# Performance work log

Measured on AMD Instinct MI355X. Metric: run time of the kernel, lower is better.

Reference implementation:

```python
import jax, jax.numpy as jnp
import numpy as np

EPS = 1e-5

def layer_norm(x, w, b):
    m = jnp.mean(x, axis=-1, keepdims=True)
    v = jnp.mean(jnp.square(x - m), axis=-1, keepdims=True)
    return (x - m) * jax.lax.rsqrt(v + EPS) * w + b

def setup_inputs() -> dict:
    key = jax.random.key(0)
    B, S, D, H = 4, 2048, 768, 12
    Dh, F = D // H, 4 * D
    ks = jax.random.split(key, 16)
    s = 0.02
    return {
        "x":    jax.random.normal(ks[0], (B, S, D), dtype=jnp.float32),
        # per-head q/k/v projections stacked over heads: [H, D, Dh]
        "Wq":   jax.random.normal(ks[1], (H, D, Dh), dtype=jnp.float32) * s,
        "bq":   jnp.zeros((H, Dh), dtype=jnp.float32),
        "Wk":   jax.random.normal(ks[2], (H, D, Dh), dtype=jnp.float32) * s,
        "bk":   jnp.zeros((H, Dh), dtype=jnp.float32),
        "Wv":   jax.random.normal(ks[3], (H, D, Dh), dtype=jnp.float32) * s,
        "bv":   jnp.zeros((H, Dh), dtype=jnp.float32),
        "Wo":   jax.random.normal(ks[4], (D, D), dtype=jnp.float32) * s,
        "bo":   jnp.zeros((D,), dtype=jnp.float32),
        "W1":   jax.random.normal(ks[5], (D, F), dtype=jnp.float32) * s,
        "b1":   jnp.zeros((F,), dtype=jnp.float32),
        "W2":   jax.random.normal(ks[6], (F, D), dtype=jnp.float32) * s,
        "b2":   jnp.zeros((D,), dtype=jnp.float32),
        "ln1_w": jnp.ones((D,), dtype=jnp.float32),
        "ln1_b": jnp.zeros((D,), dtype=jnp.float32),
        "ln2_w": jnp.ones((D,), dtype=jnp.float32),
        "ln2_b": jnp.zeros((D,), dtype=jnp.float32),
    }

def reference(x, Wq, bq, Wk, bk, Wv, bv, Wo, bo, W1, b1, W2, b2,
              ln1_w, ln1_b, ln2_w, ln2_b):
    B, S, D = x.shape
    H, _, Dh = Wq.shape
    scale = jnp.sqrt(jnp.float32(Dh))  # torch scales by sqrt(dout)
    # q,k,v: [B, H, S, Dh]
    q = jnp.einsum('bsd,hde->bhse', x, Wq) + bq[None, :, None, :]
    k = jnp.einsum('bsd,hde->bhse', x, Wk) + bk[None, :, None, :]
    v = jnp.einsum('bsd,hde->bhse', x, Wv) + bv[None, :, None, :]
    scores = jnp.einsum('bhqe,bhke->bhqk', q, k) / scale  # [B,H,S,S]
    causal = jnp.tril(jnp.ones((S, S), dtype=bool))
    scores = jnp.where(causal[None, None], scores, -jnp.inf)
    attn = jax.nn.softmax(scores, axis=-1)
    ctx = jnp.einsum('bhqk,bhke->bhqe', attn, v)           # [B,H,S,Dh]
    ctx = jnp.transpose(ctx, (0, 2, 1, 3)).reshape(B, S, D)  # concat heads
    att_out = ctx @ Wo + bo
    h = layer_norm(x + att_out, ln1_w, ln1_b)  # post-norm, dropout=0
    ff = jax.nn.gelu(h @ W1 + b1, approximate=False) @ W2 + b2
    return layer_norm(h + ff, ln2_w, ln2_b)
```

## Files before the change

### kernel.cpp

```cpp
#include <hip/hip_runtime.h>
#include <hip/hip_bf16.h>
#include <math.h>

#define B_ 4
#define S_ 2048
#define D_ 768
#define H_ 12
#define DH_ 64
#define F_ 3072
#define NTOK (B_*S_)
#define BH_ (B_*H_)

typedef __hip_bfloat16 bf16;
typedef __attribute__((ext_vector_type(8))) short bf16x8;
typedef __attribute__((ext_vector_type(4))) float f32x4;
typedef __attribute__((ext_vector_type(4))) _Float16 half4;
typedef __attribute__((ext_vector_type(8))) _Float16 half8;

#define GLD16(g, l) __builtin_amdgcn_global_load_lds( \
    (__attribute__((address_space(1))) void*)(uintptr_t)(g), \
    (__attribute__((address_space(3))) void*)(uintptr_t)(l), 16, 0, 0)

__device__ __forceinline__ float bs2f(short s){
  union { unsigned int u; float f; } cv; cv.u = ((unsigned int)(unsigned short)s) << 16; return cv.f;
}
__device__ __forceinline__ float b2f(bf16 v){ return __bfloat162float(v); }
__device__ __forceinline__ bf16 f2b(float v){ return __float2bfloat16(v); }
__device__ __forceinline__ short f2bb(float v){ bf16 b = f2b(v); short s; __builtin_memcpy(&s, &b, 2); return s; }

__device__ __forceinline__ float gelu_fast(float v){
  const float c0 = -2.302208157f;
  const float c1 = -0.102943238f;
  float w = v*v;
  float z = v * __builtin_fmaf(c1, w, c0);
  float t = __builtin_amdgcn_exp2f(z);
  return v * __builtin_amdgcn_rcpf(1.0f + t);
}

__global__ void f32_to_bf16_k(const float* __restrict__ in, bf16* __restrict__ out, int n){
  int i = blockIdx.x*256 + threadIdx.x;
  if (i < n) out[i] = f2b(in[i]);
}

__global__ __launch_bounds__(256) void transpose_f32_bf16_k(const float* __restrict__ in,
    bf16* __restrict__ out, int K, int N){
  __shared__ float t[32][33];
  const int kb = blockIdx.y*32, nb = blockIdx.x*32;
  const int x = threadIdx.x & 31, y = threadIdx.x >> 5;
#pragma unroll
  for (int yy = y; yy < 32; yy += 8)
    t[yy][x] = in[(size_t)(kb+yy)*N + nb + x];
  __syncthreads();
#pragma unroll
  for (int yy = y; yy < 32; yy += 8)
    out[(size_t)(nb+yy)*K + kb + x] = f2b(t[x][yy]);
}

__global__ void pack_qkv_t_k(const float* __restrict__ Wq, const float* __restrict__ bq,
                             const float* __restrict__ Wk, const float* __restrict__ bk,
                             const float* __restrict__ Wv, const float* __restrict__ bv,
                             bf16* __restrict__ Wt, float* __restrict__ bcat){
  int idx = blockIdx.x*256 + threadIdx.x;
  if (idx < 3*D_*D_){
    int n = idx / D_;
    int k = idx - n*D_;
    int which = n / D_;
    int cc = n - which*D_;
    int h = cc >> 6, e = cc & 63;
    const float* W = (which==0) ? Wq : ((which==1) ? Wk : Wv);
    Wt[idx] = f2b(W[((size_t)h*D_ + k)*DH_ + e]);
  }
  if (idx < 3*D_){
    int which = idx / D_;
    int cc = idx - which*D_;
    int h = cc >> 6, e = cc & 63;
    const float* bb = (which==0) ? bq : ((which==1) ? bk : bv);
    bcat[idx] = bb[h*DH_ + e];
  }
}

template<int EPI>
__global__ __launch_bounds__(256) void mgemm_k(
    const bf16* __restrict__ A, const bf16* __restrict__ Bt,
    const float* __restrict__ bias, const bf16* __restrict__ aux,
    bf16* __restrict__ C, int M, int N, int K,
    bf16* __restrict__ qb, bf16* __restrict__ kbuf, _Float16* __restrict__ vt)
{
  __shared__ bf16 As[4096];
  __shared__ bf16 Bs[4096];
  const int tid  = threadIdx.x;
  const int wave = tid >> 6, lane = tid & 63;
  const int quad = lane >> 4, l16 = lane & 15;
  const int wm = (wave >> 1) * 64, wn = (wave & 1) * 64;

  const int NX = gridDim.x;
  const int f  = blockIdx.y * NX + blockIdx.x;
  const int xcd = f & 7;
  const int j   = f >> 3;
  const int bx  = j % NX;
  const int by  = (j / NX) * 8 + xcd;
  const int m0 = by * 128, n0 = bx * 128;

  const int srow  = lane >> 2;
  const int schunk = (lane & 3) ^ ((srow >> 1) & 3);
  const bf16* gA0 = A  + (size_t)(m0 + wave*16 + srow)*K + schunk*8;
  const bf16* gA1 = gA0 + (size_t)64*K;
  const bf16* gB0 = Bt + (size_t)(n0 + wave*16 + srow)*K + schunk*8;
  const bf16* gB1 = gB0 + (size_t)64*K;
  const uintptr_t asb = (uintptr_t)(void*)As + (size_t)wave*1024;
  const uintptr_t bsb = (uintptr_t)(void*)Bs + (size_t)wave*1024;

  f32x4 acc[4][4];
#pragma unroll
  for (int i=0;i<4;i++)
#pragma unroll
    for (int j2=0;j2<4;j2++) acc[i][j2] = (f32x4)0.f;

  const char* AsB = (const char*)As;
  const char* BsB = (const char*)Bs;
  const int fsw = (quad ^ ((l16 >> 1) & 3)) * 16;

  for (int k0 = 0; k0 < K; k0 += 32){
    __syncthreads();
    GLD16(gA0, asb);
    GLD16(gA1, asb + 4096);
    GLD16(gB0, bsb);
    GLD16(gB1, bsb + 4096);
    gA0 += 32; gA1 += 32; gB0 += 32; gB1 += 32;
    __syncthreads();
    bf16x8 af[4], bfr[4];
#pragma unroll
    for (int i=0;i<4;i++) af[i]  = *(const bf16x8*)(AsB + ((wm + i*16 + l16) << 6) + fsw);
#pragma unroll
    for (int j2=0;j2<4;j2++) bfr[j2] = *(const bf16x8*)(BsB + ((wn + j2*16 + l16) << 6) + fsw);
#pragma unroll
    for (int i=0;i<4;i++)
#pragma unroll
      for (int j2=0;j2<4;j2++)
        acc[i][j2] = __builtin_amdgcn_mfma_f32_16x16x32_bf16(af[i], bfr[j2], acc[i][j2], 0, 0, 0);
  }

#pragma unroll
  for (int i=0;i<4;i++){
#pragma unroll
    for (int j2=0;j2<4;j2++){
      const int n = n0 + wn + j2*16 + l16;
      const int m_base = m0 + wm + i*16 + quad*4;
      if (EPI == 0){
        const int which = n / D_;
        const int cc = n - which*D_;
        const int h = cc >> 6, e = cc & 63;
        if (which == 2){
          const int b = m_base >> 11, s = m_base & (S_-1);
          const int sl = s & 63;
          const int perm = ((sl>>2)&3)*16 + ((sl>>4)&3)*4;
          half4 hv;
#pragma unroll
          for (int r=0;r<4;r++) hv[r] = (_Float16)(acc[i][j2][r] + bias[n]);
          *(half4*)(vt + ((size_t)(b*H_+h)*DH_ + e)*S_ + (s & ~63) + perm) = hv;
        } else {
          bf16* dst = (which==0) ? qb : kbuf;
          const float sc2 = (which==0) ? 0.125f : 1.0f;
#pragma unroll
          for (int r=0;r<4;r++){
            const int m = m_base + r;
            const int b = m >> 11, s = m & (S_-1);
            dst[((size_t)(b*H_+h)*S_ + s)*DH_ + e] = f2b((acc[i][j2][r] + bias[n]) * sc2);
          }
        }
      } else {
#pragma unroll
        for (int r=0;r<4;r++){
          const int m = m_base + r;
          float v = acc[i][j2][r] + bias[n];
          if (EPI == 1){
            v += b2f(aux[(size_t)m*N + n]);
            C[(size_t)m*N + n] = f2b(v);
          } else {
            C[(size_t)m*N + n] = f2b(gelu_fast(v));
          }
        }
      }
    }
  }
}

__global__ __launch_bounds__(256) void mgemm64_k(
    const bf16* __restrict__ A, const bf16* __restrict__ Bt,
    const float* __restrict__ bias, const bf16* __restrict__ aux,
    bf16* __restrict__ C, int M, int N, int K)
{
  __shared__ bf16 As[4096];
  __shared__ bf16 Bs[8192];
  const int tid  = threadIdx.x;
  const int wave = tid >> 6, lane = tid & 63;
  const int quad = lane >> 4, l16 = lane & 15;
  const int wm = (wave >> 1) * 32, wn = (wave & 1) * 64;

  const int NX = gridDim.x;
  const int f  = blockIdx.y * NX + blockIdx.x;
  const int xcd = f & 7;
  const int j   = f >> 3;
  const int bx  = j % NX;
  const int by  = (j / NX) * 8 + xcd;
  const int m0 = by * 64, n0 = bx * 128;

  const int srow8 = lane >> 3;
  const int g     = (lane & 7) ^ srow8;
  const bf16* gA0 = A  + (size_t)(m0 + wave*16 +      srow8)*K + g*8;
  const bf16* gA1 = A  + (size_t)(m0 + wave*16 +  8 + srow8)*K + g*8;
  const bf16* gB0 = Bt + (size_t)(n0 + wave*32 +      srow8)*K + g*8;
  const bf16* gB1 = Bt + (size_t)(n0 + wave*32 +  8 + srow8)*K + g*8;
  const bf16* gB2 = Bt + (size_t)(n0 + wave*32 + 16 + srow8)*K + g*8;
  const bf16* gB3 = Bt + (size_t)(n0 + wave*32 + 24 + srow8)*K + g*8;
  const uintptr_t asb = (uintptr_t)(void*)As + (size_t)wave*16*128;
  const uintptr_t bsb = (uintptr_t)(void*)Bs + (size_t)wave*32*128;

  f32x4 acc[2][4];
#pragma unroll
  for (int i=0;i<2;i++)
#pragma unroll
    for (int j2=0;j2<4;j2++) acc[i][j2] = (f32x4)0.f;

  const char* AsB = (const char*)As;
  const char* BsB = (const char*)Bs;

  for (int k0 = 0; k0 < K; k0 += 64){
    __syncthreads();
    GLD16(gA0, asb);
    GLD16(gA1, asb + 1024);
    GLD16(gB0, bsb);
    GLD16(gB1, bsb + 1024);
    GLD16(gB2, bsb + 2048);
    GLD16(gB3, bsb + 3072);
    gA0 += 64; gA1 += 64; gB0 += 64; gB1 += 64; gB2 += 64; gB3 += 64;
    __syncthreads();
#pragma unroll
    for (int kq = 0; kq < 2; kq++){
      const int cbase = kq*4 + quad;
      bf16x8 af[2], bfr[4];
#pragma unroll
      for (int i=0;i<2;i++){
        const int m = wm + i*16 + l16;
        af[i] = *(const bf16x8*)(AsB + (m << 7) + ((cbase ^ (m & 7)) << 4));
      }
#pragma unroll
      for (int j2=0;j2<4;j2++){
        const int n = wn + j2*16 + l16;
        bfr[j2] = *(const bf16x8*)(BsB + (n << 7) + ((cbase ^ (n & 7)) << 4));
      }
#pragma unroll
      for (int i=0;i<2;i++)
#pragma unroll
        for (int j2=0;j2<4;j2++)
          acc[i][j2] = __builtin_amdgcn_mfma_f32_16x16x32_bf16(af[i], bfr[j2], acc[i][j2], 0, 0, 0);
    }
  }

#pragma unroll
  for (int i=0;i<2;i++){
#pragma unroll
    for (int j2=0;j2<4;j2++){
      const int n = n0 + wn + j2*16 + l16;
      const int m_base = m0 + wm + i*16 + quad*4;
#pragma unroll
      for (int r=0;r<4;r++){
        const int m = m_base + r;
        float v = acc[i][j2][r] + bias[n] + b2f(aux[(size_t)m*N + n]);
        C[(size_t)m*N + n] = f2b(v);
      }
    }
  }
}

__global__ __launch_bounds__(256) void fattn_k(const bf16* __restrict__ qb,
    const bf16* __restrict__ kb, const _Float16* __restrict__ vt, bf16* __restrict__ ctx)
{
  __shared__ __align__(16) char smem[19456];
  bf16     (*Ks)[72] = (bf16(*)[72])smem;
  _Float16 (*Vs)[72] = (_Float16(*)[72])(smem + 9216);
  float* maxb  = (float*)(smem + 18432);
  float* libuf = (float*)(smem + 18944);
  float* Obuf  = (float*)smem;

  const int bh = blockIdx.x;
  const int qt = 31 - blockIdx.y;
  const int q0 = qt * 64;
  const int tid = threadIdx.x;
  const int wave = tid >> 6, lane = tid & 63;
  const int quad = lane >> 4, l16 = lane & 15;
  const int kh = wave >> 1, qh = wave & 1;
  const size_t kbase = (size_t)bh * S_ * DH_;

  bf16x8 qf[2][2];
#pragma unroll
  for (int nf=0; nf<2; nf++)
#pragma unroll
    for (int h=0; h<2; h++)
      qf[nf][h] = *(const bf16x8*)(qb + kbase + (size_t)(q0 + qh*32 + nf*16 + l16)*DH_ + h*32 + quad*8);

  f32x4 o[4][2];
#pragma unroll
  for (int df=0; df<4; df++){ o[df][0] = (f32x4)0.f; o[df][1] = (f32x4)0.f; }
  float mi[2] = {-1e30f, -1e30f}, li[2] = {0.f, 0.f};

  for (int kt = 0; kt <= qt; ++kt){
    const int k0 = kt * 64;
    __syncthreads();
    {
      const int r = tid >> 2, seg = (tid & 3) * 16;
      const bf16* ksrc = kb + kbase + (size_t)(k0 + r)*DH_ + seg;
      bf16x8 ka = *(const bf16x8*)ksrc;
      bf16x8 kc2 = *(const bf16x8*)(ksrc + 8);
      *(bf16x8*)&Ks[r][seg]   = ka;
      *(bf16x8*)&Ks[r][seg+8] = kc2;
      const _Float16* vsrc = vt + ((size_t)bh*DH_ + r)*S_ + k0 + seg;
      half8 va = *(const half8*)vsrc;
      half8 vb2 = *(const half8*)(vsrc + 8);
      *(half8*)&Vs[r][seg]   = va;
      *(half8*)&Vs[r][seg+8] = vb2;
    }
    __syncthreads();

    bf16x8 af[2][2];
#pragma unroll
    for (int mf=0; mf<2; mf++)
#pragma unroll
      for (int h=0; h<2; h++)
        af[mf][h] = *(const bf16x8*)&Ks[kh*32 + mf*16 + l16][h*32 + quad*8];
    f32x4 sc[2][2];
#pragma unroll
    for (int mf=0; mf<2; mf++)
#pragma unroll
      for (int nf=0; nf<2; nf++){
        f32x4 t = __builtin_amdgcn_mfma_f32_16x16x32_bf16(af[mf][0], qf[nf][0], (f32x4)0.f, 0, 0, 0);
        sc[mf][nf] = __builtin_amdgcn_mfma_f32_16x16x32_bf16(af[mf][1], qf[nf][1], t, 0, 0, 0);
      }

    if (kt == qt){
#pragma unroll
      for (int mf=0; mf<2; mf++){
        const int keyl = kh*32 + mf*16 + quad*4;
#pragma unroll
        for (int nf=0; nf<2; nf++){
          const int ql = qh*32 + nf*16 + l16;
#pragma unroll
          for (int r=0; r<4; r++)
            if (keyl + r > ql) sc[mf][nf][r] = -1e30f;
        }
      }
    }

    float mw[2];
#pragma unroll
    for (int nf=0; nf<2; nf++){
      float mx = -1e30f;
#pragma unroll
      for (int mf=0; mf<2; mf++)
#pragma unroll
        for (int r=0; r<4; r++) mx = fmaxf(mx, sc[mf][nf][r]);
      mx = fmaxf(mx, __shfl_xor(mx, 16));
      mx = fmaxf(mx, __shfl_xor(mx, 32));
      mw[nf] = mx;
    }
    if (quad == 0){
      maxb[kh*64 + qh*32 + l16]      = mw[0];
      maxb[kh*64 + qh*32 + 16 + l16] = mw[1];
    }
    __syncthreads();

    half4 pf[2][2];
    float alpha[2];
#pragma unroll
    for (int nf=0; nf<2; nf++){
      const float mo = maxb[(1-kh)*64 + qh*32 + nf*16 + l16];
      const float mn = fmaxf(mi[nf], fmaxf(mw[nf], mo));
      alpha[nf] = __expf(mi[nf] - mn);
      mi[nf] = mn;
      float rs = 0.f;
#pragma unroll
      for (int mf=0; mf<2; mf++)
#pragma unroll
        for (int r=0; r<4; r++){
          float p = __expf(sc[mf][nf][r] - mn);
          pf[mf][nf][r] = (_Float16)p;
          rs += p;
        }
      rs += __shfl_xor(rs, 16);
      rs += __shfl_xor(rs, 32);
      li[nf] = li[nf]*alpha[nf] + rs;
    }

#pragma unroll
    for (int df=0; df<4; df++)
#pragma unroll
      for (int nf=0; nf<2; nf++)
#pragma unroll
        for (int r=0; r<4; r++) o[df][nf][r] *= alpha[nf];

#pragma unroll
    for (int df=0; df<4; df++){
      half8 vv = *(const half8*)&Vs[df*16 + l16][quad*16 + kh*8];
      half4 vlo = __builtin_shufflevector(vv, vv, 0,1,2,3);
      half4 vhi = __builtin_shufflevector(vv, vv, 4,5,6,7);
#pragma unroll
      for (int nf=0; nf<2; nf++){
        o[df][nf] = __builtin_amdgcn_mfma_f32_16x16x16f16(vlo, pf[0][nf], o[df][nf], 0, 0, 0);
        o[df][nf] = __builtin_amdgcn_mfma_f32_16x16x16f16(vhi, pf[1][nf], o[df][nf], 0, 0, 0);
      }
    }
  }

  __syncthreads();
  if (quad == 0){
    libuf[kh*64 + qh*32 + l16]      = li[0];
    libuf[kh*64 + qh*32 + 16 + l16] = li[1];
  }
  if (kh == 1){
#pragma unroll
    for (int df=0; df<4; df++)
#pragma unroll
      for (int nf=0; nf<2; nf++)
#pragma unroll
        for (int r=0; r<4; r++)
          Obuf[(qh*64 + df*16 + quad*4 + r)*33 + nf*16 + l16] = o[df][nf][r];
  }
  __syncthreads();
  if (kh == 0){
    const int b = bh / H_, h = bh - (bh / H_)*H_;
#pragma unroll
    for (int nf=0; nf<2; nf++){
      const int q64 = qh*32 + nf*16 + l16;
      const float inv = 1.0f / (libuf[q64] + libuf[64 + q64]);
      const int qtok = q0 + q64;
#pragma unroll
      for (int df=0; df<4; df++){
        short4 pk;
        float v0 = (o[df][nf][0] + Obuf[(qh*64 + df*16 + quad*4 + 0)*33 + nf*16 + l16]) * inv;
        float v1 = (o[df][nf][1] + Obuf[(qh*64 + df*16 + quad*4 + 1)*33 + nf*16 + l16]) * inv;
        float v2 = (o[df][nf][2] + Obuf[(qh*64 + df*16 + quad*4 + 2)*33 + nf*16 + l16]) * inv;
        float v3 = (o[df][nf][3] + Obuf[(qh*64 + df*16 + quad*4 + 3)*33 + nf*16 + l16]) * inv;
        pk.x = f2bb(v0); pk.y = f2bb(v1); pk.z = f2bb(v2); pk.w = f2bb(v3);
        *(short4*)((short*)ctx + ((size_t)(b*S_ + qtok))*D_ + h*DH_ + df*16 + quad*4) = pk;
      }
    }
  }
}

template<typename T> __device__ __forceinline__ void stf(T* p, float v);
template<> __device__ __forceinline__ void stf<float>(float* p, float v){ *p = v; }
template<> __device__ __forceinline__ void stf<bf16>(bf16* p, float v){ *p = f2b(v); }

template<typename OutT>
__global__ __launch_bounds__(256) void layernorm_k(const bf16* __restrict__ X,
    const float* __restrict__ g, const float* __restrict__ bta, OutT* __restrict__ Y)
{
  const int row = blockIdx.x;
  const int tid = threadIdx.x;
  const bf16* xr = X + (size_t)row * D_;
  float vals[3];
  float s = 0.f, s2 = 0.f;
#pragma unroll
  for (int i = 0; i < 3; i++){
    float v = b2f(xr[tid + i*256]);
    vals[i] = v; s += v; s2 += v*v;
  }
#pragma unroll
  for (int o = 32; o > 0; o >>= 1){ s += __shfl_down(s, o); s2 += __shfl_down(s2, o); }
  __shared__ float rs[4], rq[4];
  const int lane = tid & 63, w = tid >> 6;
  if (lane == 0){ rs[w] = s; rq[w] = s2; }
  __syncthreads();
  s  = rs[0]+rs[1]+rs[2]+rs[3];
  s2 = rq[0]+rq[1]+rq[2]+rq[3];
  const float mean = s * (1.0f/D_);
  const float var  = s2 * (1.0f/D_) - mean*mean;
  const float inv  = rsqrtf(var + 1e-5f);
#pragma unroll
  for (int i = 0; i < 3; i++){
    int c = tid + i*256;
    float o = (vals[i] - mean) * inv * g[c] + bta[c];
    stf(Y + (size_t)row*D_ + c, o);
  }
}

extern "C" void kernel_launch(void* const* d_in, const int* in_sizes, int n_in,
                              void* d_out, int out_size, void* d_ws, size_t ws_size,
                              hipStream_t stream)
{
  const float* x   = (const float*)d_in[0];
  const float* Wq  = (const float*)d_in[1];
  const float* bq  = (const float*)d_in[2];
  const float* Wk  = (const float*)d_in[3];
  const float* bk  = (const float*)d_in[4];
  const float* Wv  = (const float*)d_in[5];
  const float* bv  = (const float*)d_in[6];
  const float* Wo  = (const float*)d_in[7];
  const float* bo  = (const float*)d_in[8];
  const float* W1  = (const float*)d_in[9];
  const float* b1  = (const float*)d_in[10];
  const float* W2  = (const float*)d_in[11];
  const float* b2  = (const float*)d_in[12];
  const float* g1  = (const float*)d_in[13];
  const float* be1 = (const float*)d_in[14];
  const float* g2  = (const float*)d_in[15];
  const float* be2 = (const float*)d_in[16];
  float* out = (float*)d_out;

  char* ws = (char*)d_ws;
  size_t off = 0;
  auto alloc = [&](size_t bytes)->char*{
    char* p = ws + off; off = (off + bytes + 255) & ~(size_t)255; return p;
  };
  bf16*  xb    = (bf16*) alloc((size_t)NTOK*D_*2);
  bf16*  WcatT = (bf16*) alloc((size_t)3*D_*D_*2);
  float* bcat  = (float*)alloc((size_t)3*D_*4);
  bf16*  WoT   = (bf16*) alloc((size_t)D_*D_*2);
  bf16*  W1T   = (bf16*) alloc((size_t)F_*D_*2);
  bf16*  W2T   = (bf16*) alloc((size_t)D_*F_*2);
  bf16*  r1    = (bf16*) alloc((size_t)NTOK*F_*2);
  bf16*  qb    = r1;
  bf16*  kb    = r1 + (size_t)NTOK*D_;
  _Float16* vt = (_Float16*)(r1 + (size_t)2*NTOK*D_);
  bf16*  ff1   = r1;
  bf16*  ctxb  = (bf16*) alloc((size_t)NTOK*D_*2);
  bf16*  y1    = (bf16*) alloc((size_t)NTOK*D_*2);
  bf16*  hb    = (bf16*) alloc((size_t)NTOK*D_*2);
  bf16*  y2    = ctxb;

  f32_to_bf16_k<<<(NTOK*D_+255)/256, 256, 0, stream>>>(x, xb, NTOK*D_);
  transpose_f32_bf16_k<<<dim3(D_/32, D_/32), 256, 0, stream>>>(Wo, WoT, D_, D_);
  transpose_f32_bf16_k<<<dim3(F_/32, D_/32), 256, 0, stream>>>(W1, W1T, D_, F_);
  transpose_f32_bf16_k<<<dim3(D_/32, F_/32), 256, 0, stream>>>(W2, W2T, F_, D_);
  pack_qkv_t_k<<<(3*D_*D_+255)/256, 256, 0, stream>>>(Wq,bq,Wk,bk,Wv,bv,WcatT,bcat);

  mgemm_k<0><<<dim3(3*D_/128, NTOK/128), 256, 0, stream>>>(
      xb, WcatT, bcat, nullptr, nullptr, NTOK, 3*D_, D_, qb, kb, vt);

  fattn_k<<<dim3(BH_, S_/64), 256, 0, stream>>>(qb, kb, vt, ctxb);

  mgemm64_k<<<dim3(D_/128, NTOK/64), 256, 0, stream>>>(
      ctxb, WoT, bo, xb, y1, NTOK, D_, D_);

  layernorm_k<bf16><<<NTOK, 256, 0, stream>>>(y1, g1, be1, hb);

  mgemm_k<2><<<dim3(F_/128, NTOK/128), 256, 0, stream>>>(
      hb, W1T, b1, nullptr, ff1, NTOK, F_, D_, nullptr, nullptr, nullptr);

  mgemm64_k<<<dim3(D_/128, NTOK/64), 256, 0, stream>>>(
      ff1, W2T, b2, hb, y2, NTOK, D_, F_);

  layernorm_k<float><<<NTOK, 256, 0, stream>>>(y2, g2, be2, out);
}
```

Measured before the change: 412.7 us.

## Replace 128x128 GEMM with double-buffered 256x256 tile kernel using interleaved prefetch

The QKV projection and FFN1 GEMMs now use a 512-thread kernel computing 256x256 output tiles with BK=64, double-buffered LDS, and async global-to-LDS prefetch of the next k-tile interleaved between MFMA phases. Barriers are raw s_barrier, and s_setprio raises wave priority during MFMA bursts. The intent is to raise arithmetic intensity per block and overlap memory loads with compute instead of syncing twice per 32-wide k step. The cost is 128 KB of LDS and more accumulator registers per thread, which may limit occupancy. Grid granularity also gets coarser (9x32 and 12x32 blocks).

After: 410.3 us. Within noise of the previous version (-0.6%).

```diff
diff --git a/kernel.cpp b/kernel.cpp
--- a/kernel.cpp
+++ b/kernel.cpp
@@ -27,6 +27,11 @@
 __device__ __forceinline__ float b2f(bf16 v){ return __bfloat162float(v); }
 __device__ __forceinline__ bf16 f2b(float v){ return __float2bfloat16(v); }
 __device__ __forceinline__ short f2bb(float v){ bf16 b = f2b(v); short s; __builtin_memcpy(&s, &b, 2); return s; }
+
+__device__ __forceinline__ void wgbar(){
+  __builtin_amdgcn_s_barrier();
+  asm volatile("" ::: "memory");
+}
 
 __device__ __forceinline__ float gelu_fast(float v){
   const float c0 = -2.302208157f;
@@ -79,69 +84,130 @@
   }
 }
 
+#define STAGE_A(bufi_, kh_, kt_) do { \
+    GLD16(gA  + (size_t)(kt_)*64 + (kh_)*32, asb + ((bufi_)<<15) + ((kh_)<<14)); \
+    GLD16(gA2 + (size_t)(kt_)*64 + (kh_)*32, asb + ((bufi_)<<15) + ((kh_)<<14) + 8192); } while(0)
+#define STAGE_B(bufi_, kh_, kt_) do { \
+    GLD16(gB  + (size_t)(kt_)*64 + (kh_)*32, bsb + ((bufi_)<<15) + ((kh_)<<14)); \
+    GLD16(gB2 + (size_t)(kt_)*64 + (kh_)*32, bsb + ((bufi_)<<15) + ((kh_)<<14) + 8192); } while(0)
+#define AFRAG(bufi_, ks_, i_) (*(const bf16x8*)(AsB + ((bufi_)<<15) + ((ks_)<<14) + ((wm + (i_)*16 + l16)<<6) + fsw))
+#define BFRAG(bufi_, ks_, j_) (*(const bf16x8*)(BsB + ((bufi_)<<15) + ((ks_)<<14) + ((wn + (j_)*16 + l16)<<6) + fsw))
+
 template<int EPI>
-__global__ __launch_bounds__(256) void mgemm_k(
+__global__ __launch_bounds__(512, 2) void mgemm256_k(
     const bf16* __restrict__ A, const bf16* __restrict__ Bt,
-    const float* __restrict__ bias, const bf16* __restrict__ aux,
-    bf16* __restrict__ C, int M, int N, int K,
+    const float* __restrict__ bias, bf16* __restrict__ C,
+    int M, int N, int K,
     bf16* __restrict__ qb, bf16* __restrict__ kbuf, _Float16* __restrict__ vt)
 {
-  __shared__ bf16 As[4096];
-  __shared__ bf16 Bs[4096];
+  __shared__ __align__(16) bf16 As[32768];
+  __shared__ __align__(16) bf16 Bs[32768];
   const int tid  = threadIdx.x;
   const int wave = tid >> 6, lane = tid & 63;
   const int quad = lane >> 4, l16 = lane & 15;
-  const int wm = (wave >> 1) * 64, wn = (wave & 1) * 64;
+  const int wm = (wave >> 2) * 128;
+  const int wn = (wave & 3) * 64;
 
   const int NX = gridDim.x;
   const int f  = blockIdx.y * NX + blockIdx.x;
   const int xcd = f & 7;
-  const int j   = f >> 3;
-  const int bx  = j % NX;
-  const int by  = (j / NX) * 8 + xcd;
-  const int m0 = by * 128, n0 = bx * 128;
-
-  const int srow  = lane >> 2;
-  const int schunk = (lane & 3) ^ ((srow >> 1) & 3);
-  const bf16* gA0 = A  + (size_t)(m0 + wave*16 + srow)*K + schunk*8;
-  const bf16* gA1 = gA0 + (size_t)64*K;
-  const bf16* gB0 = Bt + (size_t)(n0 + wave*16 + srow)*K + schunk*8;
-  const bf16* gB1 = gB0 + (size_t)64*K;
+  const int j0  = f >> 3;
+  const int bx  = j0 % NX;
+  const int by  = (j0 / NX) * 8 + xcd;
+  const int m0 = by * 256, n0 = bx * 256;
+
+  const int srow = tid >> 2;
+  const int sg   = (tid & 3) ^ ((tid >> 3) & 3);
+  const bf16* gA  = A  + (size_t)(m0 + srow)*K + sg*8;
+  const bf16* gA2 = A  + (size_t)(m0 + 128 + srow)*K + sg*8;
+  const bf16* gB  = Bt + (size_t)(n0 + srow)*K + sg*8;
+  const bf16* gB2 = Bt + (size_t)(n0 + 128 + srow)*K + sg*8;
   const uintptr_t asb = (uintptr_t)(void*)As + (size_t)wave*1024;
   const uintptr_t bsb = (uintptr_t)(void*)Bs + (size_t)wave*1024;
-
-  f32x4 acc[4][4];
-#pragma unroll
-  for (int i=0;i<4;i++)
-#pragma unroll
-    for (int j2=0;j2<4;j2++) acc[i][j2] = (f32x4)0.f;
 
   const char* AsB = (const char*)As;
   const char* BsB = (const char*)Bs;
   const int fsw = (quad ^ ((l16 >> 1) & 3)) * 16;
 
-  for (int k0 = 0; k0 < K; k0 += 32){
-    __syncthreads();
-    GLD16(gA0, asb);
-    GLD16(gA1, asb + 4096);
-    GLD16(gB0, bsb);
-    GLD16(gB1, bsb + 4096);
-    gA0 += 32; gA1 += 32; gB0 += 32; gB1 += 32;
-    __syncthreads();
+  f32x4 acc[8][4];
+#pragma unroll
+  for (int i=0;i<8;i++)
+#pragma unroll
+    for (int j2=0;j2<4;j2++) acc[i][j2] = (f32x4)0.f;
+
+  const int KT = K >> 6;
+
+  STAGE_A(0, 0, 0); STAGE_B(0, 0, 0); STAGE_A(0, 1, 0); STAGE_B(0, 1, 0);
+  asm volatile("s_waitcnt vmcnt(4)" ::: "memory");
+  wgbar();
+
+  for (int kt = 0; kt < KT; ++kt){
+    const int bufc = kt & 1, bufn = bufc ^ 1;
+    const bool pf = (kt + 1) < KT;
     bf16x8 af[4], bfr[4];
-#pragma unroll
-    for (int i=0;i<4;i++) af[i]  = *(const bf16x8*)(AsB + ((wm + i*16 + l16) << 6) + fsw);
-#pragma unroll
-    for (int j2=0;j2<4;j2++) bfr[j2] = *(const bf16x8*)(BsB + ((wn + j2*16 + l16) << 6) + fsw);
+
+#pragma unroll
+    for (int i=0;i<4;i++) af[i] = AFRAG(bufc, 0, i);
+#pragma unroll
+    for (int j2=0;j2<4;j2++) bfr[j2] = BFRAG(bufc, 0, j2);
+    if (pf) STAGE_A(bufn, 0, kt+1);
+    wgbar();
+    __builtin_amdgcn_s_setprio(1);
 #pragma unroll
     for (int i=0;i<4;i++)
 #pragma unroll
       for (int j2=0;j2<4;j2++)
         acc[i][j2] = __builtin_amdgcn_mfma_f32_16x16x32_bf16(af[i], bfr[j2], acc[i][j2], 0, 0, 0);
-  }
-
-#pragma unroll
-  for (int i=0;i<4;i++){
+    __builtin_amdgcn_s_setprio(0);
+    wgbar();
+
+#pragma unroll
+    for (int i=0;i<4;i++) af[i] = AFRAG(bufc, 0, 4+i);
+    if (pf) STAGE_B(bufn, 0, kt+1);
+    wgbar();
+    __builtin_amdgcn_s_setprio(1);
+#pragma unroll
+    for (int i=0;i<4;i++)
+#pragma unroll
+      for (int j2=0;j2<4;j2++)
+        acc[4+i][j2] = __builtin_amdgcn_mfma_f32_16x16x32_bf16(af[i], bfr[j2], acc[4+i][j2], 0, 0, 0);
+    __builtin_amdgcn_s_setprio(0);
+    if (pf) asm volatile("s_waitcnt vmcnt(4)" ::: "memory");
+    else    asm volatile("s_waitcnt vmcnt(0)" ::: "memory");
+    wgbar();
+
+#pragma unroll
+    for (int i=0;i<4;i++) af[i] = AFRAG(bufc, 1, i);
+#pragma unroll
+    for (int j2=0;j2<4;j2++) bfr[j2] = BFRAG(bufc, 1, j2);
+    if (pf) STAGE_A(bufn, 1, kt+1);
+    wgbar();
+    __builtin_amdgcn_s_setprio(1);
+#pragma unroll
+    for (int i=0;i<4;i++)
+#pragma unroll
+      for (int j2=0;j2<4;j2++)
+        acc[i][j2] = __builtin_amdgcn_mfma_f32_16x16x32_bf16(af[i], bfr[j2], acc[i][j2], 0, 0, 0);
+    __builtin_amdgcn_s_setprio(0);
+    wgbar();
+
+#pragma unroll
+    for (int i=0;i<4;i++) af[i] = AFRAG(bufc, 1, 4+i);
+    if (pf) STAGE_B(bufn, 1, kt+1);
+    wgbar();
+    __builtin_amdgcn_s_setprio(1);
+#pragma unroll
+    for (int i=0;i<4;i++)
+#pragma unroll
+      for (int j2=0;j2<4;j2++)
+        acc[4+i][j2] = __builtin_amdgcn_mfma_f32_16x16x32_bf16(af[i], bfr[j2], acc[4+i][j2], 0, 0, 0);
+    __builtin_amdgcn_s_setprio(0);
+    if (pf) asm volatile("s_waitcnt vmcnt(4)" ::: "memory");
+    wgbar();
+  }
+
+#pragma unroll
+  for (int i=0;i<8;i++){
 #pragma unroll
     for (int j2=0;j2<4;j2++){
       const int n = n0 + wn + j2*16 + l16;
@@ -173,17 +239,16 @@
         for (int r=0;r<4;r++){
           const int m = m_base + r;
           float v = acc[i][j2][r] + bias[n];
-          if (EPI == 1){
-            v += b2f(aux[(size_t)m*N + n]);
-            C[(size_t)m*N + n] = f2b(v);
-          } else {
-            C[(size_t)m*N + n] = f2b(gelu_fast(v));
-          }
+          C[(size_t)m*N + n] = f2b(gelu_fast(v));
         }
       }
     }
   }
 }
+#undef STAGE_A
+#undef STAGE_B
+#undef AFRAG
+#undef BFRAG
 
 __global__ __launch_bounds__(256) void mgemm64_k(
     const bf16* __restrict__ A, const bf16* __restrict__ Bt,
@@ -534,8 +599,8 @@
   transpose_f32_bf16_k<<<dim3(D_/32, F_/32), 256, 0, stream>>>(W2, W2T, F_, D_);
   pack_qkv_t_k<<<(3*D_*D_+255)/256, 256, 0, stream>>>(Wq,bq,Wk,bk,Wv,bv,WcatT,bcat);
 
-  mgemm_k<0><<<dim3(3*D_/128, NTOK/128), 256, 0, stream>>>(
-      xb, WcatT, bcat, nullptr, nullptr, NTOK, 3*D_, D_, qb, kb, vt);
+  mgemm256_k<0><<<dim3(3*D_/256, NTOK/256), 512, 0, stream>>>(
+      xb, WcatT, bcat, nullptr, NTOK, 3*D_, D_, qb, kb, vt);
 
   fattn_k<<<dim3(BH_, S_/64), 256, 0, stream>>>(qb, kb, vt, ctxb);
 
@@ -544,8 +609,8 @@
 
   layernorm_k<bf16><<<NTOK, 256, 0, stream>>>(y1, g1, be1, hb);
 
-  mgemm_k<2><<<dim3(F_/128, NTOK/128), 256, 0, stream>>>(
-      hb, W1T, b1, nullptr, ff1, NTOK, F_, D_, nullptr, nullptr, nullptr);
+  mgemm256_k<2><<<dim3(F_/256, NTOK/256), 512, 0, stream>>>(
+      hb, W1T, b1, ff1, NTOK, F_, D_, nullptr, nullptr, nullptr);
 
   mgemm64_k<<<dim3(D_/128, NTOK/64), 256, 0, stream>>>(
       ff1, W2T, b2, hb, y2, NTOK, D_, F_);
```
